# Kernel optimization log

Measured on AMD Instinct MI355X. Metric: run time of the kernel, lower is better.

## Reference

```python
import jax, jax.numpy as jnp
import numpy as np

N_NODES = 20000
N_EDGES = 640000
FEAT = 128


def setup_inputs() -> dict:
    key = jax.random.key(0)
    k1, k2, k3, k4 = jax.random.split(key, 4)
    x = jax.random.normal(k1, (1, N_NODES, FEAT, 4), dtype=jnp.float32)
    edge_index = jax.random.randint(k2, (2, N_EDGES), 0, N_NODES, dtype=jnp.int64)
    # Linear(in_channels=128, out_channels=128): W [out, in], b [out]
    W = jax.random.normal(k3, (FEAT, FEAT), dtype=jnp.float32) * 0.05
    b = jax.random.normal(k4, (FEAT,), dtype=jnp.float32) * 0.05
    return {"x": x, "edge_index": edge_index, "W": W, "b": b}


def reference(x, edge_index, W, b):
    # x: [B, N, F, T]
    B, N, F, T = x.shape
    # permute -> [B, T, N, F]; Linear over feature dim (out == in == F)
    h = jnp.einsum('bnft,of->btno', x, W) + b          # [B, T, N, F]
    h = h.reshape(B * T, N, F)                          # flatten batch*time
    src = edge_index[0]  # message source (x_j)
    dst = edge_index[1]  # scatter target
    msgs = h[:, src, :]                                 # [B*T, E, F] gather
    # scatter-max per target node (PyG aggr='max'); vmap over batch*time
    agg = jax.vmap(lambda m: jax.ops.segment_max(m, dst, num_segments=N))(msgs)
    # nodes with no incoming edges: segment_max yields -inf -> 0 (PyG fill)
    agg = jnp.where(jnp.isneginf(agg), jnp.zeros_like(agg), agg)
    out = agg.reshape(B, T, N, F).transpose(0, 2, 3, 1)  # [B, N, F, T]
    return out
```

## Files before the change

### kernel.cpp

```cpp
#include <hip/hip_runtime.h>
#include <hip/hip_bf16.h>
#include <stdint.h>

#define N_NODES 20000
#define N_EDGES 640000
#define FEAT 128
#define CAPD 128
#define NPHASE 8

typedef __attribute__((ext_vector_type(8))) short bf16x8;
typedef __attribute__((ext_vector_type(4))) float f32x4;

__device__ __forceinline__ unsigned short bf16r(float f) {
  unsigned a = __float_as_uint(f);
  a = (a + 0x7FFFu + ((a >> 16) & 1u)) >> 16;
  return (unsigned short)a;
}

__device__ __forceinline__ unsigned pkbf16(float lo, float hi) {
  __hip_bfloat162 p = __float22bfloat162_rn(make_float2(lo, hi));
  return *reinterpret_cast<unsigned*>(&p);
}

__device__ __forceinline__ void mx2(unsigned u, float& a, float& b) {
  a = fmaxf(a, __uint_as_float(u << 16));
  b = fmaxf(b, __uint_as_float(u & 0xFFFF0000u));
}

#define MX4(v)                                           \
  do {                                                   \
    mx2((v).x, m0, m1); mx2((v).y, m2, m3);              \
    mx2((v).z, m4, m5); mx2((v).w, m6, m7);              \
  } while (0)

__global__ void init_kernel(const float* __restrict__ W,
                            unsigned short* __restrict__ Wbf,
                            int* __restrict__ cnt) {
  int i = blockIdx.x * 256 + threadIdx.x;
  if (i < N_NODES) cnt[i] = 0;
  if (i < FEAT * FEAT / 2) {
    float2 w = ((const float2*)W)[i];
    ((unsigned*)Wbf)[i] = pkbf16(w.x, w.y);
  }
}

__global__ __launch_bounds__(256) void gemm_scatter_kernel(
    const float4* __restrict__ x, const unsigned short* __restrict__ Wbf,
    const float* __restrict__ b, uint4* __restrict__ h,
    const int* __restrict__ ei, int* __restrict__ cnt,
    unsigned short* __restrict__ csr) {
  __shared__ __align__(16) unsigned short sm[17408 / 2];
  const int tid = threadIdx.x;
  const int n0 = blockIdx.x * 16;

#pragma unroll
  for (int it = 0; it < 4; ++it) {
    int e = tid + it * 256;
    int n = e >> 6, fp = e & 63;
    float4 a = x[(size_t)(n0 + n) * 128 + 2 * fp];
    float4 c = x[(size_t)(n0 + n) * 128 + 2 * fp + 1];
    ((unsigned*)sm)[(0 * 16 + n) * 68 + fp] = pkbf16(a.x, c.x);
    ((unsigned*)sm)[(1 * 16 + n) * 68 + fp] = pkbf16(a.y, c.y);
    ((unsigned*)sm)[(2 * 16 + n) * 68 + fp] = pkbf16(a.z, c.z);
    ((unsigned*)sm)[(3 * 16 + n) * 68 + fp] = pkbf16(a.w, c.w);
  }

#pragma unroll
  for (int r = 0; r < 2; ++r) {
    int e = blockIdx.x * 512 + r * 256 + tid;
    int src = ei[e];
    int dst = ei[N_EDGES + e];
    int pos = atomicAdd(&cnt[dst], 1);
    if (pos < CAPD) csr[(size_t)dst * CAPD + pos] = (unsigned short)src;
  }

  __syncthreads();

  const int wv = tid >> 6;
  const int l = tid & 63;
  const int col = l & 15;
  const int quad = l >> 4;

  f32x4 acc[8];
#pragma unroll
  for (int os = 0; os < 8; ++os) {
    float bv = b[os * 16 + col];
    acc[os] = (f32x4){bv, bv, bv, bv};
  }

#pragma unroll
  for (int k = 0; k < 4; ++k) {
    bf16x8 af = *(const bf16x8*)&sm[(wv * 16 + col) * 136 + k * 32 + quad * 8];
#pragma unroll
    for (int os = 0; os < 8; ++os) {
      bf16x8 bfv = *(const bf16x8*)&Wbf[(os * 16 + col) * 128 + k * 32 + quad * 8];
      acc[os] = __builtin_amdgcn_mfma_f32_16x16x32_bf16(af, bfv, acc[os], 0, 0, 0);
    }
  }

  __syncthreads();

#pragma unroll
  for (int os = 0; os < 8; ++os) {
#pragma unroll
    for (int r = 0; r < 4; ++r) {
      sm[(quad * 4 + r) * 520 + (os * 16 + col) * 4 + wv] = bf16r(acc[os][r]);
    }
  }
  __syncthreads();

#pragma unroll
  for (int it = 0; it < 4; ++it) {
    int e = tid + it * 256;
    int n = e >> 6, q = e & 63;
    uint4 v = *(const uint4*)&sm[n * 520 + q * 8];
    h[(size_t)(n0 + n) * 64 + q] = v;
  }
}

__global__ __launch_bounds__(256) void agg_kernel(
    const uint4* __restrict__ h, const int* __restrict__ cnt,
    const unsigned short* __restrict__ csr, float4* __restrict__ out) {
  const int p = blockIdx.y;
  const int w = threadIdx.x >> 6;
  const int lane = threadIdx.x & 63;
  const int n = blockIdx.x * 4 + w;
  const int sub = lane >> 3;
  const int oq = lane & 7;

  int e1 = (int)csr[(size_t)n * CAPD + lane];
  int e2 = (int)csr[(size_t)n * CAPD + 64 + lane];
  int deg = cnt[n];
  deg = deg > CAPD ? CAPD : deg;
  int idx0 = __shfl(e1, 0);

  float m0 = -INFINITY, m1 = m0, m2 = m0, m3 = m0, m4 = m0, m5 = m0, m6 = m0, m7 = m0;

  const size_t pbase = (size_t)p * 8 + oq;
  int ngrp = (deg + 7) >> 3;
  int g = 0;
  for (; g + 2 <= ngrp; g += 2) {
    int s0 = g * 8 + sub;
    int s1 = s0 + 8;
    int srcA = __shfl((g < 8) ? e1 : e2, s0 & 63);
    int srcB = __shfl((g + 1 < 8) ? e1 : e2, s1 & 63);
    srcA = (s0 < deg) ? srcA : idx0;
    srcB = (s1 < deg) ? srcB : idx0;
    uint4 vA = h[(size_t)srcA * 64 + pbase];
    uint4 vB = h[(size_t)srcB * 64 + pbase];
    MX4(vA);
    MX4(vB);
  }
  if (g < ngrp) {
    int s0 = g * 8 + sub;
    int src = __shfl((g < 8) ? e1 : e2, s0 & 63);
    src = (s0 < deg) ? src : idx0;
    uint4 v = h[(size_t)src * 64 + pbase];
    MX4(v);
  }

#pragma unroll
  for (int d = 8; d <= 32; d <<= 1) {
    m0 = fmaxf(m0, __shfl_xor(m0, d));
    m1 = fmaxf(m1, __shfl_xor(m1, d));
    m2 = fmaxf(m2, __shfl_xor(m2, d));
    m3 = fmaxf(m3, __shfl_xor(m3, d));
    m4 = fmaxf(m4, __shfl_xor(m4, d));
    m5 = fmaxf(m5, __shfl_xor(m5, d));
    m6 = fmaxf(m6, __shfl_xor(m6, d));
    m7 = fmaxf(m7, __shfl_xor(m7, d));
  }
  if (deg == 0) {
    m0 = m1 = m2 = m3 = m4 = m5 = m6 = m7 = 0.0f;
  }
  if (lane < 8) {
    out[(size_t)n * 128 + p * 16 + lane * 2] = make_float4(m0, m1, m2, m3);
    out[(size_t)n * 128 + p * 16 + lane * 2 + 1] = make_float4(m4, m5, m6, m7);
  }
}

extern "C" void kernel_launch(void* const* d_in, const int* in_sizes, int n_in,
                              void* d_out, int out_size, void* d_ws, size_t ws_size,
                              hipStream_t stream) {
  const float* x = (const float*)d_in[0];
  const int* ei = (const int*)d_in[1];
  const float* W = (const float*)d_in[2];
  const float* b = (const float*)d_in[3];
  float* out = (float*)d_out;

  char* ws = (char*)d_ws;
  uint4* h = (uint4*)ws;
  int* cnt = (int*)(ws + 20480000);
  unsigned short* csr = (unsigned short*)(ws + 20560000);
  unsigned short* Wbf = (unsigned short*)(ws + 25680000);

  init_kernel<<<(N_NODES + 255) / 256, 256, 0, stream>>>(W, Wbf, cnt);
  gemm_scatter_kernel<<<N_NODES / 16, 256, 0, stream>>>((const float4*)x, Wbf, b, h,
                                                        ei, cnt, csr);
  agg_kernel<<<dim3(N_NODES / 4, NPHASE), 256, 0, stream>>>(h, cnt, csr, (float4*)out);
}
```

Measured before the change: 200.8 us.

## Use order-preserving 16-bit encoding with packed u16 max; split scatter kernel; flatten agg grid

Stores the GEMM output as an order-preserving unsigned 16-bit encoding of bf16, so the aggregation can take the max with packed v_pk_max_u16 on two features per instruction instead of unpacking to floats and calling fmaxf. The shuffle reduction also runs on four packed registers instead of eight floats, and decoding happens once at output. It also moves the edge-scatter CSR build into its own kernel and flattens the agg grid so the phase index cycles fastest, which may improve cache locality on gathered rows. The extra kernel launch and the encode/decode work are added costs.

```diff
diff --git a/kernel.cpp b/kernel.cpp
--- a/kernel.cpp
+++ b/kernel.cpp
@@ -11,26 +11,31 @@
 typedef __attribute__((ext_vector_type(8))) short bf16x8;
 typedef __attribute__((ext_vector_type(4))) float f32x4;
 
-__device__ __forceinline__ unsigned short bf16r(float f) {
-  unsigned a = __float_as_uint(f);
-  a = (a + 0x7FFFu + ((a >> 16) & 1u)) >> 16;
-  return (unsigned short)a;
-}
-
 __device__ __forceinline__ unsigned pkbf16(float lo, float hi) {
   __hip_bfloat162 p = __float22bfloat162_rn(make_float2(lo, hi));
   return *reinterpret_cast<unsigned*>(&p);
 }
 
-__device__ __forceinline__ void mx2(unsigned u, float& a, float& b) {
-  a = fmaxf(a, __uint_as_float(u << 16));
-  b = fmaxf(b, __uint_as_float(u & 0xFFFF0000u));
-}
-
-#define MX4(v)                                           \
-  do {                                                   \
-    mx2((v).x, m0, m1); mx2((v).y, m2, m3);              \
-    mx2((v).z, m4, m5); mx2((v).w, m6, m7);              \
+__device__ __forceinline__ unsigned short enc16(float f) {
+  unsigned a = __float_as_uint(f);
+  unsigned b = (a + 0x7FFFu + ((a >> 16) & 1u)) >> 16;
+  unsigned s = (unsigned)((int)a >> 31);
+  return (unsigned short)((b ^ 0x8000u) ^ (s & 0x7FFFu));
+}
+
+__device__ __forceinline__ float dec16(unsigned e) {
+  unsigned b = (e & 0x8000u) ? (e ^ 0x8000u) : (e ^ 0xFFFFu);
+  return __uint_as_float(b << 16);
+}
+
+__device__ __forceinline__ void pmax(unsigned& a, unsigned v) {
+  asm("v_pk_max_u16 %0, %0, %1" : "+v"(a) : "v"(v));
+}
+
+#define PMX4(v)                                              \
+  do {                                                       \
+    pmax(a0, (v).x); pmax(a1, (v).y);                        \
+    pmax(a2, (v).z); pmax(a3, (v).w);                        \
   } while (0)
 
 __global__ void init_kernel(const float* __restrict__ W,
@@ -44,11 +49,19 @@
   }
 }
 
-__global__ __launch_bounds__(256) void gemm_scatter_kernel(
+__global__ __launch_bounds__(256) void scatter_kernel(const int* __restrict__ ei,
+                                                      int* __restrict__ cnt,
+                                                      unsigned short* __restrict__ csr) {
+  int e = blockIdx.x * 256 + threadIdx.x;
+  int src = ei[e];
+  int dst = ei[N_EDGES + e];
+  int pos = atomicAdd(&cnt[dst], 1);
+  if (pos < CAPD) csr[(size_t)dst * CAPD + pos] = (unsigned short)src;
+}
+
+__global__ __launch_bounds__(256) void gemm_kernel(
     const float4* __restrict__ x, const unsigned short* __restrict__ Wbf,
-    const float* __restrict__ b, uint4* __restrict__ h,
-    const int* __restrict__ ei, int* __restrict__ cnt,
-    unsigned short* __restrict__ csr) {
+    const float* __restrict__ b, uint4* __restrict__ h) {
   __shared__ __align__(16) unsigned short sm[17408 / 2];
   const int tid = threadIdx.x;
   const int n0 = blockIdx.x * 16;
@@ -65,15 +78,6 @@
     ((unsigned*)sm)[(3 * 16 + n) * 68 + fp] = pkbf16(a.w, c.w);
   }
 
-#pragma unroll
-  for (int r = 0; r < 2; ++r) {
-    int e = blockIdx.x * 512 + r * 256 + tid;
-    int src = ei[e];
-    int dst = ei[N_EDGES + e];
-    int pos = atomicAdd(&cnt[dst], 1);
-    if (pos < CAPD) csr[(size_t)dst * CAPD + pos] = (unsigned short)src;
-  }
-
   __syncthreads();
 
   const int wv = tid >> 6;
@@ -104,7 +108,7 @@
   for (int os = 0; os < 8; ++os) {
 #pragma unroll
     for (int r = 0; r < 4; ++r) {
-      sm[(quad * 4 + r) * 520 + (os * 16 + col) * 4 + wv] = bf16r(acc[os][r]);
+      sm[(quad * 4 + r) * 520 + (os * 16 + col) * 4 + wv] = enc16(acc[os][r]);
     }
   }
   __syncthreads();
@@ -121,10 +125,12 @@
 __global__ __launch_bounds__(256) void agg_kernel(
     const uint4* __restrict__ h, const int* __restrict__ cnt,
     const unsigned short* __restrict__ csr, float4* __restrict__ out) {
-  const int p = blockIdx.y;
+  const int bid = blockIdx.x;
+  const int p = bid & 7;
+  const int grp = bid >> 3;
   const int w = threadIdx.x >> 6;
   const int lane = threadIdx.x & 63;
-  const int n = blockIdx.x * 4 + w;
+  const int n = grp * 4 + w;
   const int sub = lane >> 3;
   const int oq = lane & 7;
 
@@ -134,7 +140,7 @@
   deg = deg > CAPD ? CAPD : deg;
   int idx0 = __shfl(e1, 0);
 
-  float m0 = -INFINITY, m1 = m0, m2 = m0, m3 = m0, m4 = m0, m5 = m0, m6 = m0, m7 = m0;
+  unsigned a0 = 0x007F007Fu, a1 = a0, a2 = a0, a3 = a0;
 
   const size_t pbase = (size_t)p * 8 + oq;
   int ngrp = (deg + 7) >> 3;
@@ -148,34 +154,38 @@
     srcB = (s1 < deg) ? srcB : idx0;
     uint4 vA = h[(size_t)srcA * 64 + pbase];
     uint4 vB = h[(size_t)srcB * 64 + pbase];
-    MX4(vA);
-    MX4(vB);
+    PMX4(vA);
+    PMX4(vB);
   }
   if (g < ngrp) {
     int s0 = g * 8 + sub;
     int src = __shfl((g < 8) ? e1 : e2, s0 & 63);
     src = (s0 < deg) ? src : idx0;
     uint4 v = h[(size_t)src * 64 + pbase];
-    MX4(v);
+    PMX4(v);
   }
 
 #pragma unroll
   for (int d = 8; d <= 32; d <<= 1) {
-    m0 = fmaxf(m0, __shfl_xor(m0, d));
-    m1 = fmaxf(m1, __shfl_xor(m1, d));
-    m2 = fmaxf(m2, __shfl_xor(m2, d));
-    m3 = fmaxf(m3, __shfl_xor(m3, d));
-    m4 = fmaxf(m4, __shfl_xor(m4, d));
-    m5 = fmaxf(m5, __shfl_xor(m5, d));
-    m6 = fmaxf(m6, __shfl_xor(m6, d));
-    m7 = fmaxf(m7, __shfl_xor(m7, d));
-  }
-  if (deg == 0) {
-    m0 = m1 = m2 = m3 = m4 = m5 = m6 = m7 = 0.0f;
-  }
+    pmax(a0, (unsigned)__shfl_xor((int)a0, d));
+    pmax(a1, (unsigned)__shfl_xor((int)a1, d));
+    pmax(a2, (unsigned)__shfl_xor((int)a2, d));
+    pmax(a3, (unsigned)__shfl_xor((int)a3, d));
+  }
+
   if (lane < 8) {
-    out[(size_t)n * 128 + p * 16 + lane * 2] = make_float4(m0, m1, m2, m3);
-    out[(size_t)n * 128 + p * 16 + lane * 2 + 1] = make_float4(m4, m5, m6, m7);
+    float4 o0, o1;
+    if (deg == 0) {
+      o0 = make_float4(0.f, 0.f, 0.f, 0.f);
+      o1 = o0;
+    } else {
+      o0 = make_float4(dec16(a0 & 0xFFFFu), dec16(a0 >> 16),
+                       dec16(a1 & 0xFFFFu), dec16(a1 >> 16));
+      o1 = make_float4(dec16(a2 & 0xFFFFu), dec16(a2 >> 16),
+                       dec16(a3 & 0xFFFFu), dec16(a3 >> 16));
+    }
+    out[(size_t)n * 128 + p * 16 + lane * 2] = o0;
+    out[(size_t)n * 128 + p * 16 + lane * 2 + 1] = o1;
   }
 }
 
@@ -195,7 +205,7 @@
   unsigned short* Wbf = (unsigned short*)(ws + 25680000);
 
   init_kernel<<<(N_NODES + 255) / 256, 256, 0, stream>>>(W, Wbf, cnt);
-  gemm_scatter_kernel<<<N_NODES / 16, 256, 0, stream>>>((const float4*)x, Wbf, b, h,
-                                                        ei, cnt, csr);
-  agg_kernel<<<dim3(N_NODES / 4, NPHASE), 256, 0, stream>>>(h, cnt, csr, (float4*)out);
-}
+  scatter_kernel<<<N_EDGES / 256, 256, 0, stream>>>(ei, cnt, csr);
+  gemm_kernel<<<N_NODES / 16, 256, 0, stream>>>((const float4*)x, Wbf, b, h);
+  agg_kernel<<<(N_NODES / 4) * NPHASE, 256, 0, stream>>>(h, cnt, csr, (float4*)out);
+}
```

New measurement: 203.9 us. No clear change (+1.6%).
